# Kernel optimization log

Hardware: AMD Instinct MI355X
Metric: run time of the kernel (lower is better)

Reference implementation:

```python
import jax, jax.numpy as jnp
import numpy as np

S, B, E, H = 2048, 1, 1024, 16
D = E // H                     # head_dim = 64
WINDOW = 1024                  # sliding_window_size
NEG_INF = jnp.float32(-1e30)


def setup_inputs() -> dict:
    key = jax.random.key(0)
    ks = jax.random.split(key, 8)
    w_scale = (2.0 / (E + E)) ** 0.5  # xavier_uniform-ish std
    inp = {
        "query": jax.random.normal(ks[0], (S, B, E), jnp.float32),
        "key": jax.random.normal(ks[1], (S, B, E), jnp.float32),
        "value": jax.random.normal(ks[2], (S, B, E), jnp.float32),
        "positions_bias": jax.random.normal(ks[3], (B * H, S, S), jnp.float32) * 0.1,
        "Wq": jax.random.normal(ks[4], (E, E), jnp.float32) * w_scale,
        "bq": jnp.zeros((E,), jnp.float32),
        "Wk": jax.random.normal(ks[5], (E, E), jnp.float32) * w_scale,
        "bk": jnp.zeros((E,), jnp.float32),
        "Wv": jax.random.normal(ks[6], (E, E), jnp.float32) * w_scale,
        "bv": jnp.zeros((E,), jnp.float32),
        "Wo": jax.random.normal(ks[7], (E, E), jnp.float32) * w_scale,
        "bo": jnp.zeros((E,), jnp.float32),
    }
    return inp


def _heads(x):
    # [S, B, E] -> [B, H, S, D]
    return x.reshape(S, B, H, D).transpose(1, 2, 0, 3)


def _stream(qh, kh, vh, bias, Wo, bo):
    scaling = D ** -0.5
    # NOTE: original pre-scales q by head_dim**-0.5 AND flex_attention applies
    # its default 1/sqrt(head_dim) scale -> effective q.k / head_dim.
    scores = jnp.einsum("bhqd,bhkd->bhqk", qh, kh) * scaling + bias
    qi = jnp.arange(S)[:, None]
    kj = jnp.arange(S)[None, :]
    mask = (qi >= kj) & (qi - kj <= WINDOW)  # causal + sliding window
    scores = jnp.where(mask, scores, NEG_INF)
    p = jax.nn.softmax(scores, axis=-1)
    o = jnp.einsum("bhqk,bhkd->bhqd", p, vh)
    o = o.transpose(2, 0, 1, 3).reshape(S, B, E)  # [S, B, E]
    return o @ Wo.T + bo


def reference(query, key, value, positions_bias, Wq, bq, Wk, bk, Wv, bv, Wo, bo):
    scaling = D ** -0.5
    kh = _heads(key @ Wk.T + bk)
    vh = _heads(value @ Wv.T + bv)
    # query passed as a single tensor -> c == q (non-tuple branch)
    ch = _heads((query @ Wq.T + bq) * scaling)
    bias = positions_bias.reshape(B, H, S, S)
    # content stream (attn_mask=None) and query stream (query_mask=None,
    # query_position_bias defaults to positions_bias) compute identical math
    # here since c == q; XLA will CSE the duplicate.
    c_out = _stream(ch, kh, vh, bias, Wo, bo)
    q_out = _stream(ch, kh, vh, bias, Wo, bo)
    return (c_out, q_out)
```

## Files before the change

### kernel.cpp

```cpp
#include <hip/hip_runtime.h>

typedef unsigned short u16;
typedef __bf16 bf16x8 __attribute__((ext_vector_type(8)));
typedef float f32x4 __attribute__((ext_vector_type(4)));

#define S_LEN 2048
#define EMB   1024
#define NHEAD 16
#define HDIM  64
#define WIN   1024

#define AS1 __attribute__((address_space(1)))
#define AS3 __attribute__((address_space(3)))

__device__ __forceinline__ u16 f2bf(float f) {
  unsigned u = __float_as_uint(f);
  u += 0x7FFFu + ((u >> 16) & 1u);
  return (u16)(u >> 16);
}

__global__ __launch_bounds__(256) void conv_kernel(
    const float* __restrict__ p0, const float* __restrict__ p1,
    const float* __restrict__ p2, const float* __restrict__ p3,
    const float* __restrict__ p4, const float* __restrict__ p5,
    const float* __restrict__ p6,
    u16* __restrict__ o0, u16* __restrict__ o1, u16* __restrict__ o2,
    u16* __restrict__ o3, u16* __restrict__ o4, u16* __restrict__ o5,
    u16* __restrict__ o6) {
  const float* src; u16* dst; int n;
  switch (blockIdx.y) {
    case 0: src = p0; dst = o0; n = S_LEN * EMB; break;
    case 1: src = p1; dst = o1; n = S_LEN * EMB; break;
    case 2: src = p2; dst = o2; n = S_LEN * EMB; break;
    case 3: src = p3; dst = o3; n = EMB * EMB; break;
    case 4: src = p4; dst = o4; n = EMB * EMB; break;
    case 5: src = p5; dst = o5; n = EMB * EMB; break;
    default: src = p6; dst = o6; n = EMB * EMB; break;
  }
  int i = (blockIdx.x * 256 + threadIdx.x) * 4;
  if (i >= n) return;
  float4 v = *reinterpret_cast<const float4*>(src + i);
  ushort4 r;
  r.x = f2bf(v.x); r.y = f2bf(v.y); r.z = f2bf(v.z); r.w = f2bf(v.w);
  *reinterpret_cast<ushort4*>(dst + i) = r;
}

__device__ __forceinline__ void gemm_128x64_core(
    const u16* __restrict__ A, const u16* __restrict__ W,
    const float* __restrict__ bias, float scale, int mode,
    u16* __restrict__ outB, float* __restrict__ outF0, float* __restrict__ outF1,
    int N, int K, int bm, int bn, u16* As, u16* Bs) {
  const int tid  = threadIdx.x;
  const int w    = tid >> 6;
  const int lane = tid & 63;
  const int wr = w >> 1, wc = w & 1;
  const int lr = lane & 15;
  const int ko = (lane >> 4) * 8;

  f32x4 acc[4][2];
#pragma unroll
  for (int i = 0; i < 4; ++i)
#pragma unroll
    for (int j = 0; j < 2; ++j) acc[i][j] = f32x4{0.f, 0.f, 0.f, 0.f};

  const int srow = lane >> 3;
  const int scol = (lane & 7) * 8;

  for (int k0 = 0; k0 < K; k0 += 64) {
    const u16* Ab = A + (size_t)bm * K + k0;
    const u16* Wb = W + (size_t)bn * K + k0;
#pragma unroll
    for (int c = 0; c < 4; ++c) {
      int s = w * 4 + c;
      __builtin_amdgcn_global_load_lds(
          (const AS1 void*)(Ab + (size_t)(s * 8 + srow) * K + scol),
          (AS3 void*)(As + s * 512), 16, 0, 0);
    }
#pragma unroll
    for (int c = 0; c < 2; ++c) {
      int s = w * 2 + c;
      __builtin_amdgcn_global_load_lds(
          (const AS1 void*)(Wb + (size_t)(s * 8 + srow) * K + scol),
          (AS3 void*)(Bs + s * 512), 16, 0, 0);
    }
    __syncthreads();
#pragma unroll
    for (int kk = 0; kk < 2; ++kk) {
      bf16x8 af[4], bfr[2];
#pragma unroll
      for (int mi = 0; mi < 4; ++mi)
        af[mi] = *reinterpret_cast<const bf16x8*>(&As[(wr * 64 + mi * 16 + lr) * 64 + kk * 32 + ko]);
#pragma unroll
      for (int ni = 0; ni < 2; ++ni)
        bfr[ni] = *reinterpret_cast<const bf16x8*>(&Bs[(wc * 32 + ni * 16 + lr) * 64 + kk * 32 + ko]);
#pragma unroll
      for (int mi = 0; mi < 4; ++mi)
#pragma unroll
        for (int ni = 0; ni < 2; ++ni)
          acc[mi][ni] = __builtin_amdgcn_mfma_f32_16x16x32_bf16(af[mi], bfr[ni], acc[mi][ni], 0, 0, 0);
    }
    __syncthreads();
  }

  const int cr = (lane >> 4) * 4;
  const int cc = lane & 15;

  if (mode == 2) {
#pragma unroll
    for (int mi = 0; mi < 4; ++mi) {
#pragma unroll
      for (int ni = 0; ni < 2; ++ni) {
        int d = wc * 32 + ni * 16 + cc;
        float bv = bias[bn + d];
#pragma unroll
        for (int r = 0; r < 4; ++r) {
          int rp = wr * 64 + mi * 16 + cr + r;
          As[d * 128 + (rp ^ ((d & 7) * 8))] = f2bf((acc[mi][ni][r] + bv) * scale);
        }
      }
    }
    __syncthreads();
    const int h = bn >> 6;
    u16* Vb = outB + (size_t)h * (HDIM * S_LEN);
    const int dd = tid >> 4;
    const int ch = tid & 15;
#pragma unroll
    for (int i = 0; i < 4; ++i) {
      int d = dd + i * 16;
      const u16* src = &As[d * 128 + ((ch ^ (d & 7)) * 8)];
      u16* dst = Vb + (size_t)d * S_LEN + bm + ch * 8;
      *reinterpret_cast<ushort4*>(dst)     = *reinterpret_cast<const ushort4*>(src);
      *reinterpret_cast<ushort4*>(dst + 4) = *reinterpret_cast<const ushort4*>(src + 4);
    }
    return;
  }

#pragma unroll
  for (int mi = 0; mi < 4; ++mi) {
#pragma unroll
    for (int ni = 0; ni < 2; ++ni) {
      int col = bn + wc * 32 + ni * 16 + cc;
      float bv = bias[col];
#pragma unroll
      for (int r = 0; r < 4; ++r) {
        int row = bm + wr * 64 + mi * 16 + cr + r;
        float val = (acc[mi][ni][r] + bv) * scale;
        if (mode == 1) {
          size_t idx = (size_t)(col >> 6) * (S_LEN * HDIM) + (size_t)row * HDIM + (col & 63);
          outB[idx] = f2bf(val);
        } else {
          outF0[(size_t)row * N + col] = val;
          outF1[(size_t)row * N + col] = val;
        }
      }
    }
  }
}

__device__ __forceinline__ void supertile_decode(int bx, int& bm, int& bn) {
  int sb = bx >> 4, inner = bx & 15;
  bm = ((sb >> 2) * 4 + (inner >> 2)) * 128;
  bn = ((sb & 3) * 4 + (inner & 3)) * 64;
}

__global__ __launch_bounds__(256, 4) void proj_gemm(
    const u16* __restrict__ Abase, const u16* __restrict__ Wbase,
    const float* __restrict__ b0, const float* __restrict__ b1,
    const float* __restrict__ b2, u16* __restrict__ Qp,
    u16* __restrict__ Kp, u16* __restrict__ Vt) {
  __shared__ u16 As[128 * 64];
  __shared__ u16 Bs[64 * 64];
  const int z = blockIdx.z;
  const u16* A = Abase + (size_t)z * (S_LEN * EMB);
  const u16* W = Wbase + (size_t)z * (EMB * EMB);
  const float* bias = (z == 0) ? b0 : (z == 1 ? b1 : b2);
  u16* O = (z == 0) ? Qp : (z == 1 ? Kp : Vt);
  float scale = (z == 0) ? (1.0f / 64.0f) : 1.0f;
  int bm, bn;
  supertile_decode(blockIdx.x, bm, bn);
  gemm_128x64_core(A, W, bias, scale, (z == 2) ? 2 : 1, O, nullptr, nullptr,
                   EMB, EMB, bm, bn, As, Bs);
}

__global__ __launch_bounds__(256, 4) void out_gemm(
    const u16* __restrict__ A, const u16* __restrict__ W,
    const float* __restrict__ bias, float* __restrict__ out0,
    float* __restrict__ out1) {
  __shared__ u16 As[128 * 64];
  __shared__ u16 Bs[64 * 64];
  int bm, bn;
  supertile_decode(blockIdx.x, bm, bn);
  gemm_128x64_core(A, W, bias, 1.0f, 0, nullptr, out0, out1,
                   EMB, EMB, bm, bn, As, Bs);
}

__global__ __launch_bounds__(256, 4) void attn_kernel(
    const u16* __restrict__ Qp, const u16* __restrict__ Kp,
    const u16* __restrict__ Vt, const float* __restrict__ pbias,
    u16* __restrict__ Ob) {
  __shared__ u16 KV[2][2][64 * 64];
  __shared__ u16 Pb[4][16 * 64];

  const int tid  = threadIdx.x;
  const int w    = tid >> 6;
  const int lane = tid & 63;
  const int h  = blockIdx.y;
  const int q0 = (gridDim.x - 1 - blockIdx.x) * 64;
  const int ql = lane & 15;
  const int g  = lane >> 4;
  const int qw = q0 + w * 16;
  const int qg = qw + ql;
  const int qw_hi = qw + 15;

  const u16* Kh  = Kp + (size_t)h * (S_LEN * HDIM);
  const u16* Vth = Vt + (size_t)h * (HDIM * S_LEN);

  const u16* Qrow = Qp + (size_t)h * (S_LEN * HDIM) + (size_t)qg * HDIM;
  bf16x8 qf0 = *reinterpret_cast<const bf16x8*>(&Qrow[g * 8]);
  bf16x8 qf1 = *reinterpret_cast<const bf16x8*>(&Qrow[32 + g * 8]);

  f32x4 o[4];
#pragma unroll
  for (int i = 0; i < 4; ++i) o[i] = f32x4{0.f, 0.f, 0.f, 0.f};
  float m = -1e30f, l = 0.f;

  const float* brow = pbias + (size_t)h * S_LEN * S_LEN + (size_t)qg * S_LEN + 4 * g;

  int kv_lo = q0 - WIN; if (kv_lo < 0) kv_lo = 0; kv_lo &= ~63;
  const int ntiles = ((q0 + 63 - kv_lo) >> 6) + 1;
  const int kv_last = kv_lo + (ntiles - 1) * 64;

  const int swz = (ql & 7) << 4;
  char* Prow = (char*)&Pb[w][0] + ql * 128;

  auto STAGE = [&](int buf, int kv0) {
    u16* Kd = &KV[buf][0][(w * 16) * 64];
    u16* Vd = &KV[buf][1][(w * 16) * 64];
#pragma unroll
    for (int n = 0; n < 2; ++n) {
      int r  = w * 16 + n * 8 + (lane >> 3);
      int cp = (lane & 7) ^ (r & 7);
      __builtin_amdgcn_global_load_lds(
          (const AS1 void*)(Kh + (size_t)(kv0 + r) * HDIM + cp * 8),
          (AS3 void*)(Kd + n * 512), 16, 0, 0);
      __builtin_amdgcn_global_load_lds(
          (const AS1 void*)(Vth + (size_t)r * S_LEN + kv0 + cp * 8),
          (AS3 void*)(Vd + n * 512), 16, 0, 0);
    }
  };

  STAGE(0, kv_lo);
  float4 nb[4], cb[4];
#pragma unroll
  for (int kt = 0; kt < 4; ++kt)
    nb[kt] = *reinterpret_cast<const float4*>(&brow[kv_lo + kt * 16]);
  int cur = 0;

  for (int t = 0; t < ntiles; ++t) {
    const int kv0 = kv_lo + t * 64;
    __syncthreads();
#pragma unroll
    for (int kt = 0; kt < 4; ++kt) cb[kt] = nb[kt];

    if (t + 1 < ntiles) STAGE(cur ^ 1, kv0 + 64);
    const int nxt = (kv0 + 64 <= kv_last) ? kv0 + 64 : kv0;
#pragma unroll
    for (int kt = 0; kt < 4; ++kt)
      nb[kt] = *reinterpret_cast<const float4*>(&brow[nxt + kt * 16]);

    const bool active = (kv0 <= qw_hi) && (kv0 + 63 >= qw - WIN);
    if (active) {
      const char* Kl = (const char*)&KV[cur][0][0];
      const char* Vl = (const char*)&KV[cur][1][0];

      f32x4 s[4];
#pragma unroll
      for (int kt = 0; kt < 4; ++kt) {
        bf16x8 ka = *reinterpret_cast<const bf16x8*>(Kl + (kt * 16 + ql) * 128 + ((g * 16) ^ swz));
        bf16x8 kb = *reinterpret_cast<const bf16x8*>(Kl + (kt * 16 + ql) * 128 + ((64 + g * 16) ^ swz));
        f32x4 acc = f32x4{0.f, 0.f, 0.f, 0.f};
        acc = __builtin_amdgcn_mfma_f32_16x16x32_bf16(ka, qf0, acc, 0, 0, 0);
        acc = __builtin_amdgcn_mfma_f32_16x16x32_bf16(kb, qf1, acc, 0, 0, 0);
        s[kt] = acc;
      }

      const bool full = (kv0 + 63 <= qw) && (qw_hi - kv0 <= WIN);
      float lmax = -INFINITY;
#pragma unroll
      for (int kt = 0; kt < 4; ++kt) {
        float bvr[4] = {cb[kt].x, cb[kt].y, cb[kt].z, cb[kt].w};
#pragma unroll
        for (int r = 0; r < 4; ++r) {
          int k = kv0 + kt * 16 + 4 * g + r;
          float xv = s[kt][r] + bvr[r];
          if (!full) {
            bool ok = (k <= qg) && ((qg - k) <= WIN);
            xv = ok ? xv : -INFINITY;
          }
          s[kt][r] = xv;
          lmax = fmaxf(lmax, xv);
        }
      }
      lmax = fmaxf(lmax, __shfl_xor(lmax, 16));
      lmax = fmaxf(lmax, __shfl_xor(lmax, 32));
      float mn = fmaxf(m, lmax);
      float corr = __expf(m - mn);
      m = mn;
      float ls = 0.f;
#pragma unroll
      for (int kt = 0; kt < 4; ++kt)
#pragma unroll
        for (int r = 0; r < 4; ++r) {
          float e = __expf(s[kt][r] - mn);
          s[kt][r] = e;
          ls += e;
        }
      ls += __shfl_xor(ls, 16);
      ls += __shfl_xor(ls, 32);
      l = l * corr + ls;
#pragma unroll
      for (int dt = 0; dt < 4; ++dt) {
        f32x4 tt = o[dt];
#pragma unroll
        for (int r = 0; r < 4; ++r) tt[r] *= corr;
        o[dt] = tt;
      }

#pragma unroll
      for (int kt = 0; kt < 4; ++kt) {
        ushort4 pw;
        pw.x = f2bf(s[kt][0]); pw.y = f2bf(s[kt][1]);
        pw.z = f2bf(s[kt][2]); pw.w = f2bf(s[kt][3]);
        *reinterpret_cast<ushort4*>(Prow + ((kt * 32 + g * 8) ^ swz)) = pw;
      }
#pragma unroll
      for (int kb = 0; kb < 2; ++kb) {
        bf16x8 pf = *reinterpret_cast<const bf16x8*>(Prow + ((kb * 64 + g * 16) ^ swz));
#pragma unroll
        for (int dt = 0; dt < 4; ++dt) {
          bf16x8 vf = *reinterpret_cast<const bf16x8*>(Vl + (dt * 16 + ql) * 128 + ((kb * 64 + g * 16) ^ swz));
          o[dt] = __builtin_amdgcn_mfma_f32_16x16x32_bf16(vf, pf, o[dt], 0, 0, 0);
        }
      }
    }
    cur ^= 1;
  }

  float inv = (l > 0.f) ? 1.f / l : 0.f;
  u16* op = &Ob[(size_t)qg * EMB + h * HDIM];
#pragma unroll
  for (int dt = 0; dt < 4; ++dt) {
    ushort4 outv;
#pragma unroll
    for (int r = 0; r < 4; ++r) ((u16*)&outv)[r] = f2bf(o[dt][r] * inv);
    *reinterpret_cast<ushort4*>(op + dt * 16 + 4 * g) = outv;
  }
}

extern "C" void kernel_launch(void* const* d_in, const int* in_sizes, int n_in,
                              void* d_out, int out_size, void* d_ws, size_t ws_size,
                              hipStream_t stream) {
  (void)in_sizes; (void)n_in; (void)out_size; (void)ws_size;
  const float* q  = (const float*)d_in[0];
  const float* k  = (const float*)d_in[1];
  const float* v  = (const float*)d_in[2];
  const float* pb = (const float*)d_in[3];
  const float* Wq = (const float*)d_in[4];
  const float* bq = (const float*)d_in[5];
  const float* Wk = (const float*)d_in[6];
  const float* bk = (const float*)d_in[7];
  const float* Wv = (const float*)d_in[8];
  const float* bv = (const float*)d_in[9];
  const float* Wo = (const float*)d_in[10];
  const float* bo = (const float*)d_in[11];
  float* out = (float*)d_out;

  const size_t SE = (size_t)S_LEN * EMB;
  const size_t EE = (size_t)EMB * EMB;
  u16* ws  = (u16*)d_ws;
  u16* qb  = ws;
  u16* kb  = qb + SE;
  u16* vb  = kb + SE;
  u16* wqb = vb + SE;
  u16* wkb = wqb + EE;
  u16* wvb = wkb + EE;
  u16* wob = wvb + EE;
  u16* Qp  = wob + EE;
  u16* Kp  = Qp + SE;
  u16* Vt  = Kp + SE;
  u16* Ob  = Vt + SE;

  conv_kernel<<<dim3(2048, 7), 256, 0, stream>>>(q, k, v, Wq, Wk, Wv, Wo,
                                                 qb, kb, vb, wqb, wkb, wvb, wob);
  proj_gemm<<<dim3(256, 1, 3), 256, 0, stream>>>(qb, wqb, bq, bk, bv, Qp, Kp, Vt);
  attn_kernel<<<dim3(32, 16), 256, 0, stream>>>(Qp, Kp, Vt, pb, Ob);
  out_gemm<<<dim3(256), 256, 0, stream>>>(Ob, wob, bo, out, out + SE);
}
```

Before: 98.54 us.

## Split KV tiles across two wave groups per block and merge softmax states

Doubles the attention block to 512 threads: two groups of four waves each take alternating KV tiles for the same 64 query rows, each with its own double-buffered K/V LDS region. At the end, group 1 writes its partial output, max and sum to LDS, and group 0 rescales and combines them before writing bf16 output. This halves the serial KV-loop length per query tile to add parallelism on the 512-block grid. The cost is double the LDS, a combine step with extra syncs, and possibly lower occupancy.

```diff
diff --git a/kernel.cpp b/kernel.cpp
--- a/kernel.cpp
+++ b/kernel.cpp
@@ -194,21 +194,23 @@
                    EMB, EMB, bm, bn, As, Bs);
 }
 
-__global__ __launch_bounds__(256, 4) void attn_kernel(
+__global__ __launch_bounds__(512, 4) void attn_kernel(
     const u16* __restrict__ Qp, const u16* __restrict__ Kp,
     const u16* __restrict__ Vt, const float* __restrict__ pbias,
     u16* __restrict__ Ob) {
-  __shared__ u16 KV[2][2][64 * 64];
-  __shared__ u16 Pb[4][16 * 64];
+  __shared__ u16 KV[2][2][2][64 * 64];
+  __shared__ u16 Pb[8][16 * 64];
 
   const int tid  = threadIdx.x;
   const int w    = tid >> 6;
+  const int g2   = w >> 2;
+  const int wg   = w & 3;
   const int lane = tid & 63;
   const int h  = blockIdx.y;
   const int q0 = (gridDim.x - 1 - blockIdx.x) * 64;
   const int ql = lane & 15;
   const int g  = lane >> 4;
-  const int qw = q0 + w * 16;
+  const int qw = q0 + wg * 16;
   const int qg = qw + ql;
   const int qw_hi = qw + 15;
 
@@ -227,18 +229,18 @@
   const float* brow = pbias + (size_t)h * S_LEN * S_LEN + (size_t)qg * S_LEN + 4 * g;
 
   int kv_lo = q0 - WIN; if (kv_lo < 0) kv_lo = 0; kv_lo &= ~63;
-  const int ntiles = ((q0 + 63 - kv_lo) >> 6) + 1;
-  const int kv_last = kv_lo + (ntiles - 1) * 64;
+  const int ntiles  = ((q0 + 63 - kv_lo) >> 6) + 1;
+  const int maxiter = (ntiles + 1) >> 1;
 
   const int swz = (ql & 7) << 4;
   char* Prow = (char*)&Pb[w][0] + ql * 128;
 
   auto STAGE = [&](int buf, int kv0) {
-    u16* Kd = &KV[buf][0][(w * 16) * 64];
-    u16* Vd = &KV[buf][1][(w * 16) * 64];
+    u16* Kd = &KV[g2][buf][0][(wg * 16) * 64];
+    u16* Vd = &KV[g2][buf][1][(wg * 16) * 64];
 #pragma unroll
     for (int n = 0; n < 2; ++n) {
-      int r  = w * 16 + n * 8 + (lane >> 3);
+      int r  = wg * 16 + n * 8 + (lane >> 3);
       int cp = (lane & 7) ^ (r & 7);
       __builtin_amdgcn_global_load_lds(
           (const AS1 void*)(Kh + (size_t)(kv0 + r) * HDIM + cp * 8),
@@ -249,29 +251,32 @@
     }
   };
 
-  STAGE(0, kv_lo);
+  const int kv_first = kv_lo + ((g2 < ntiles) ? g2 * 64 : 0);
+  STAGE(0, kv_first);
   float4 nb[4], cb[4];
 #pragma unroll
   for (int kt = 0; kt < 4; ++kt)
-    nb[kt] = *reinterpret_cast<const float4*>(&brow[kv_lo + kt * 16]);
+    nb[kt] = *reinterpret_cast<const float4*>(&brow[kv_first + kt * 16]);
   int cur = 0;
 
-  for (int t = 0; t < ntiles; ++t) {
-    const int kv0 = kv_lo + t * 64;
+  for (int i = 0; i < maxiter; ++i) {
+    const int tg  = g2 + 2 * i;
+    const int kv0 = kv_lo + tg * 64;
     __syncthreads();
 #pragma unroll
     for (int kt = 0; kt < 4; ++kt) cb[kt] = nb[kt];
 
-    if (t + 1 < ntiles) STAGE(cur ^ 1, kv0 + 64);
-    const int nxt = (kv0 + 64 <= kv_last) ? kv0 + 64 : kv0;
+    const bool havenext = (tg + 2 < ntiles);
+    if (havenext) STAGE(cur ^ 1, kv0 + 128);
+    const int nxt = havenext ? kv0 + 128 : kv_first;
 #pragma unroll
     for (int kt = 0; kt < 4; ++kt)
       nb[kt] = *reinterpret_cast<const float4*>(&brow[nxt + kt * 16]);
 
-    const bool active = (kv0 <= qw_hi) && (kv0 + 63 >= qw - WIN);
+    const bool active = (tg < ntiles) && (kv0 <= qw_hi) && (kv0 + 63 >= qw - WIN);
     if (active) {
-      const char* Kl = (const char*)&KV[cur][0][0];
-      const char* Vl = (const char*)&KV[cur][1][0];
+      const char* Kl = (const char*)&KV[g2][cur][0][0];
+      const char* Vl = (const char*)&KV[g2][cur][1][0];
 
       f32x4 s[4];
 #pragma unroll
@@ -346,14 +351,36 @@
     cur ^= 1;
   }
 
-  float inv = (l > 0.f) ? 1.f / l : 0.f;
-  u16* op = &Ob[(size_t)qg * EMB + h * HDIM];
-#pragma unroll
-  for (int dt = 0; dt < 4; ++dt) {
-    ushort4 outv;
-#pragma unroll
-    for (int r = 0; r < 4; ++r) ((u16*)&outv)[r] = f2bf(o[dt][r] * inv);
-    *reinterpret_cast<ushort4*>(op + dt * 16 + 4 * g) = outv;
+  __syncthreads();
+  float* Om = (float*)&KV[0][0][0][0];
+  if (g2 == 1) {
+    float* row = &Om[(size_t)(wg * 16 + ql) * 68];
+#pragma unroll
+    for (int dt = 0; dt < 4; ++dt)
+#pragma unroll
+      for (int r = 0; r < 4; ++r)
+        row[dt * 16 + 4 * g + r] = o[dt][r];
+    if (g == 0) { row[64] = m; row[65] = l; }
+  }
+  __syncthreads();
+  if (g2 == 0) {
+    const float* row = &Om[(size_t)(wg * 16 + ql) * 68];
+    float m1 = row[64], l1 = row[65];
+    float M  = fmaxf(m, m1);
+    float w0 = __expf(m - M), w1 = __expf(m1 - M);
+    float L  = l * w0 + l1 * w1;
+    float inv = (L > 0.f) ? 1.f / L : 0.f;
+    u16* op = &Ob[(size_t)qg * EMB + h * HDIM];
+#pragma unroll
+    for (int dt = 0; dt < 4; ++dt) {
+      ushort4 outv;
+#pragma unroll
+      for (int r = 0; r < 4; ++r) {
+        float val = (o[dt][r] * w0 + row[dt * 16 + 4 * g + r] * w1) * inv;
+        ((u16*)&outv)[r] = f2bf(val);
+      }
+      *reinterpret_cast<ushort4*>(op + dt * 16 + 4 * g) = outv;
+    }
   }
 }
 
@@ -393,6 +420,6 @@
   conv_kernel<<<dim3(2048, 7), 256, 0, stream>>>(q, k, v, Wq, Wk, Wv, Wo,
                                                  qb, kb, vb, wqb, wkb, wvb, wob);
   proj_gemm<<<dim3(256, 1, 3), 256, 0, stream>>>(qb, wqb, bq, bk, bv, Qp, Kp, Vt);
-  attn_kernel<<<dim3(32, 16), 256, 0, stream>>>(Qp, Kp, Vt, pb, Ob);
+  attn_kernel<<<dim3(32, 16), 512, 0, stream>>>(Qp, Kp, Vt, pb, Ob);
   out_gemm<<<dim3(256), 256, 0, stream>>>(Ob, wob, bo, out, out + SE);
 }
```

Measured after the change: 101.1 us. +2.6%, slower.

## Fuse fp32-to-bf16 conversion into GEMM tile loads, drop conversion kernel

Applied to the files above, without the earlier changes.

Removes the separate conversion kernel that turned the inputs and weights into bf16 copies. The projection and output GEMMs now read fp32 directly through registers, convert to bf16 in-kernel and store to LDS. This saves one launch and the write and re-read of the bf16 copies. In exchange, each GEMM reads twice the bytes per tile, loses the async global_load_lds path for fp32 operands, and uses more registers.

```diff
diff --git a/kernel.cpp b/kernel.cpp
--- a/kernel.cpp
+++ b/kernel.cpp
@@ -3,6 +3,7 @@
 typedef unsigned short u16;
 typedef __bf16 bf16x8 __attribute__((ext_vector_type(8)));
 typedef float f32x4 __attribute__((ext_vector_type(4)));
+typedef float f32x8 __attribute__((ext_vector_type(8)));
 
 #define S_LEN 2048
 #define EMB   1024
@@ -19,34 +20,9 @@
   return (u16)(u >> 16);
 }
 
-__global__ __launch_bounds__(256) void conv_kernel(
-    const float* __restrict__ p0, const float* __restrict__ p1,
-    const float* __restrict__ p2, const float* __restrict__ p3,
-    const float* __restrict__ p4, const float* __restrict__ p5,
-    const float* __restrict__ p6,
-    u16* __restrict__ o0, u16* __restrict__ o1, u16* __restrict__ o2,
-    u16* __restrict__ o3, u16* __restrict__ o4, u16* __restrict__ o5,
-    u16* __restrict__ o6) {
-  const float* src; u16* dst; int n;
-  switch (blockIdx.y) {
-    case 0: src = p0; dst = o0; n = S_LEN * EMB; break;
-    case 1: src = p1; dst = o1; n = S_LEN * EMB; break;
-    case 2: src = p2; dst = o2; n = S_LEN * EMB; break;
-    case 3: src = p3; dst = o3; n = EMB * EMB; break;
-    case 4: src = p4; dst = o4; n = EMB * EMB; break;
-    case 5: src = p5; dst = o5; n = EMB * EMB; break;
-    default: src = p6; dst = o6; n = EMB * EMB; break;
-  }
-  int i = (blockIdx.x * 256 + threadIdx.x) * 4;
-  if (i >= n) return;
-  float4 v = *reinterpret_cast<const float4*>(src + i);
-  ushort4 r;
-  r.x = f2bf(v.x); r.y = f2bf(v.y); r.z = f2bf(v.z); r.w = f2bf(v.w);
-  *reinterpret_cast<ushort4*>(dst + i) = r;
-}
-
 __device__ __forceinline__ void gemm_128x64_core(
-    const u16* __restrict__ A, const u16* __restrict__ W,
+    const u16* __restrict__ Ab16, const float* __restrict__ Af32,
+    const u16* __restrict__ Wb16, const float* __restrict__ Wf32,
     const float* __restrict__ bias, float scale, int mode,
     u16* __restrict__ outB, float* __restrict__ outF0, float* __restrict__ outF1,
     int N, int K, int bm, int bn, u16* As, u16* Bs) {
@@ -67,21 +43,64 @@
   const int scol = (lane & 7) * 8;
 
   for (int k0 = 0; k0 < K; k0 += 64) {
-    const u16* Ab = A + (size_t)bm * K + k0;
-    const u16* Wb = W + (size_t)bn * K + k0;
-#pragma unroll
-    for (int c = 0; c < 4; ++c) {
-      int s = w * 4 + c;
-      __builtin_amdgcn_global_load_lds(
-          (const AS1 void*)(Ab + (size_t)(s * 8 + srow) * K + scol),
-          (AS3 void*)(As + s * 512), 16, 0, 0);
-    }
-#pragma unroll
-    for (int c = 0; c < 2; ++c) {
-      int s = w * 2 + c;
-      __builtin_amdgcn_global_load_lds(
-          (const AS1 void*)(Wb + (size_t)(s * 8 + srow) * K + scol),
-          (AS3 void*)(Bs + s * 512), 16, 0, 0);
+    float4 av[4][2], wv[2][2];
+    if (Ab16) {
+      const u16* Ab = Ab16 + (size_t)bm * K + k0;
+#pragma unroll
+      for (int c = 0; c < 4; ++c) {
+        int s = w * 4 + c;
+        __builtin_amdgcn_global_load_lds(
+            (const AS1 void*)(Ab + (size_t)(s * 8 + srow) * K + scol),
+            (AS3 void*)(As + s * 512), 16, 0, 0);
+      }
+    } else {
+#pragma unroll
+      for (int c = 0; c < 4; ++c) {
+        int s = w * 4 + c;
+        const float* src = Af32 + (size_t)(bm + s * 8 + srow) * K + k0 + scol;
+        av[c][0] = *reinterpret_cast<const float4*>(src);
+        av[c][1] = *reinterpret_cast<const float4*>(src + 4);
+      }
+    }
+    if (Wb16) {
+      const u16* Wb = Wb16 + (size_t)bn * K + k0;
+#pragma unroll
+      for (int c = 0; c < 2; ++c) {
+        int s = w * 2 + c;
+        __builtin_amdgcn_global_load_lds(
+            (const AS1 void*)(Wb + (size_t)(s * 8 + srow) * K + scol),
+            (AS3 void*)(Bs + s * 512), 16, 0, 0);
+      }
+    } else {
+#pragma unroll
+      for (int c = 0; c < 2; ++c) {
+        int s = w * 2 + c;
+        const float* src = Wf32 + (size_t)(bn + s * 8 + srow) * K + k0 + scol;
+        wv[c][0] = *reinterpret_cast<const float4*>(src);
+        wv[c][1] = *reinterpret_cast<const float4*>(src + 4);
+      }
+    }
+    if (!Ab16) {
+#pragma unroll
+      for (int c = 0; c < 4; ++c) {
+        int s = w * 4 + c;
+        f32x8 f;
+        f[0] = av[c][0].x; f[1] = av[c][0].y; f[2] = av[c][0].z; f[3] = av[c][0].w;
+        f[4] = av[c][1].x; f[5] = av[c][1].y; f[6] = av[c][1].z; f[7] = av[c][1].w;
+        *reinterpret_cast<bf16x8*>(&As[s * 512 + lane * 8]) =
+            __builtin_convertvector(f, bf16x8);
+      }
+    }
+    if (!Wb16) {
+#pragma unroll
+      for (int c = 0; c < 2; ++c) {
+        int s = w * 2 + c;
+        f32x8 f;
+        f[0] = wv[c][0].x; f[1] = wv[c][0].y; f[2] = wv[c][0].z; f[3] = wv[c][0].w;
+        f[4] = wv[c][1].x; f[5] = wv[c][1].y; f[6] = wv[c][1].z; f[7] = wv[c][1].w;
+        *reinterpret_cast<bf16x8*>(&Bs[s * 512 + lane * 8]) =
+            __builtin_convertvector(f, bf16x8);
+      }
     }
     __syncthreads();
 #pragma unroll
@@ -164,34 +183,37 @@
 }
 
 __global__ __launch_bounds__(256, 4) void proj_gemm(
-    const u16* __restrict__ Abase, const u16* __restrict__ Wbase,
+    const float* __restrict__ qf, const float* __restrict__ kf,
+    const float* __restrict__ vf,
+    const float* __restrict__ Wqf, const float* __restrict__ Wkf,
+    const float* __restrict__ Wvf,
     const float* __restrict__ b0, const float* __restrict__ b1,
     const float* __restrict__ b2, u16* __restrict__ Qp,
     u16* __restrict__ Kp, u16* __restrict__ Vt) {
   __shared__ u16 As[128 * 64];
   __shared__ u16 Bs[64 * 64];
   const int z = blockIdx.z;
-  const u16* A = Abase + (size_t)z * (S_LEN * EMB);
-  const u16* W = Wbase + (size_t)z * (EMB * EMB);
+  const float* A = (z == 0) ? qf : (z == 1 ? kf : vf);
+  const float* W = (z == 0) ? Wqf : (z == 1 ? Wkf : Wvf);
   const float* bias = (z == 0) ? b0 : (z == 1 ? b1 : b2);
   u16* O = (z == 0) ? Qp : (z == 1 ? Kp : Vt);
   float scale = (z == 0) ? (1.0f / 64.0f) : 1.0f;
   int bm, bn;
   supertile_decode(blockIdx.x, bm, bn);
-  gemm_128x64_core(A, W, bias, scale, (z == 2) ? 2 : 1, O, nullptr, nullptr,
-                   EMB, EMB, bm, bn, As, Bs);
+  gemm_128x64_core(nullptr, A, nullptr, W, bias, scale, (z == 2) ? 2 : 1,
+                   O, nullptr, nullptr, EMB, EMB, bm, bn, As, Bs);
 }
 
 __global__ __launch_bounds__(256, 4) void out_gemm(
-    const u16* __restrict__ A, const u16* __restrict__ W,
+    const u16* __restrict__ A, const float* __restrict__ Wf,
     const float* __restrict__ bias, float* __restrict__ out0,
     float* __restrict__ out1) {
   __shared__ u16 As[128 * 64];
   __shared__ u16 Bs[64 * 64];
   int bm, bn;
   supertile_decode(blockIdx.x, bm, bn);
-  gemm_128x64_core(A, W, bias, 1.0f, 0, nullptr, out0, out1,
-                   EMB, EMB, bm, bn, As, Bs);
+  gemm_128x64_core(A, nullptr, nullptr, Wf, bias, 1.0f, 0,
+                   nullptr, out0, out1, EMB, EMB, bm, bn, As, Bs);
 }
 
 __global__ __launch_bounds__(256, 4) void attn_kernel(
@@ -376,23 +398,14 @@
   float* out = (float*)d_out;
 
   const size_t SE = (size_t)S_LEN * EMB;
-  const size_t EE = (size_t)EMB * EMB;
   u16* ws  = (u16*)d_ws;
-  u16* qb  = ws;
-  u16* kb  = qb + SE;
-  u16* vb  = kb + SE;
-  u16* wqb = vb + SE;
-  u16* wkb = wqb + EE;
-  u16* wvb = wkb + EE;
-  u16* wob = wvb + EE;
-  u16* Qp  = wob + EE;
+  u16* Qp  = ws;
   u16* Kp  = Qp + SE;
   u16* Vt  = Kp + SE;
   u16* Ob  = Vt + SE;
 
-  conv_kernel<<<dim3(2048, 7), 256, 0, stream>>>(q, k, v, Wq, Wk, Wv, Wo,
-                                                 qb, kb, vb, wqb, wkb, wvb, wob);
-  proj_gemm<<<dim3(256, 1, 3), 256, 0, stream>>>(qb, wqb, bq, bk, bv, Qp, Kp, Vt);
+  proj_gemm<<<dim3(256, 1, 3), 256, 0, stream>>>(q, k, v, Wq, Wk, Wv,
+                                                 bq, bk, bv, Qp, Kp, Vt);
   attn_kernel<<<dim3(32, 16), 256, 0, stream>>>(Qp, Kp, Vt, pb, Ob);
-  out_gemm<<<dim3(256), 256, 0, stream>>>(Ob, wob, bo, out, out + SE);
-}
+  out_gemm<<<dim3(256), 256, 0, stream>>>(Ob, Wo, bo, out, out + SE);
+}
```

Measured after the change: 116.5 us. 18.2% more time.
